# Optimization experiments

Hardware: AMD Instinct MI355X
Metric: run time of the kernel (lower is better)

The kernel has to match this reference:

```python
import math
import jax, jax.numpy as jnp
import numpy as np

N, T, F, H = 30000, 4, 128, 8  # num_node, num_type, num_fea, num_head
D = F // H


def setup_inputs() -> dict:
    key = jax.random.key(0)
    k0, k1, k2, k3, k4 = jax.random.split(key, 5)
    feature = jax.random.normal(k0, (N, F), dtype=jnp.float32)
    edge_fea = jax.random.normal(k1, (N, T, F), dtype=jnp.float32)
    node_multi_mask = jax.random.randint(k2, (N,), 0, T)
    # Xavier-uniform-like scale for [*, F, F] projection tables
    xav = math.sqrt(6.0 / (F + F))
    node_proj = jax.random.uniform(k3, (T, F, F), minval=-xav, maxval=xav, dtype=jnp.float32)
    edge_proj = jax.random.uniform(k4, (T * T, F, F), minval=-xav, maxval=xav, dtype=jnp.float32)
    return {
        "feature": feature,
        "edge_fea": edge_fea,
        "node_multi_mask": node_multi_mask,
        "node_proj": node_proj,
        "edge_proj": edge_proj,
    }


def reference(feature, edge_fea, node_multi_mask, node_proj, edge_proj):
    # Type-indexed projections. Instead of gathering per-node [F,F] matrices
    # (which would materialize N*F*F), compute projections for all T source
    # types in one batched einsum, then select each node's type with a gather.
    # node: out[n] = node_proj[mask[n]] @ feature[n]
    node_all = jnp.einsum('tgf,nf->ntg', node_proj, feature)           # [N,T,F]
    node_p = jnp.take_along_axis(node_all, node_multi_mask[:, None, None], axis=1)[:, 0]  # [N,F]
    # edge: out[n,j] = edge_proj[mask[n]*T + j] @ edge_fea[n,j]
    edge_proj_r = edge_proj.reshape(T, T, F, F)                         # [src_type, j, F, F]
    edge_all = jnp.einsum('stgf,ntf->nstg', edge_proj_r, edge_fea)      # [N,T_src,T,F]
    edge_p = jnp.take_along_axis(edge_all, node_multi_mask[:, None, None, None], axis=1)[:, 0]  # [N,T,F]

    # multi-head attention weights
    node_multi_in = node_p.reshape(N, 1, H, D).transpose(0, 2, 1, 3) / math.sqrt(D)  # [N,H,1,D]
    edge_multi_in = edge_p.reshape(N, T, H, D).transpose(0, 2, 3, 1)                  # [N,H,D,T]
    scores = jnp.matmul(node_multi_in, edge_multi_in)                                 # [N,H,1,T]
    # NOTE: original uses nn.Softmax(dim=1) -> softmax over the HEAD axis
    all_r_weight = jax.nn.softmax(scores, axis=1).transpose(0, 3, 1, 2)               # [N,T,H,1]
    return all_r_weight
```

## Files before the change

### kernel.cpp

```cpp
#include <hip/hip_runtime.h>
#include <hip/hip_bf16.h>

#define N_NODES 30000
#define T_TYPES 4
#define F_DIM   128
#define H_HEADS 8

typedef __bf16 bf16x8 __attribute__((ext_vector_type(8)));
typedef __bf16 bf16x4 __attribute__((ext_vector_type(4)));
typedef float  floatx4 __attribute__((ext_vector_type(4)));

#define WS_NPB 0
#define WS_EPB 131072

template <int CTRL>
static __device__ __forceinline__ float dpp_add(float x) {
    int xi = __builtin_bit_cast(int, x);
    int yi = __builtin_amdgcn_update_dpp(xi, xi, CTRL, 0xF, 0xF, true);
    return x + __builtin_bit_cast(float, yi);
}
static __device__ __forceinline__ float sum16(float x) {
    x = dpp_add<0xB1>(x);
    x = dpp_add<0x4E>(x);
    x = dpp_add<0x141>(x);
    x = dpp_add<0x140>(x);
    return x;
}

__global__ __launch_bounds__(256) void prep_kernel(
    const float* __restrict__ node_proj, const float* __restrict__ edge_proj,
    __bf16* __restrict__ npb, __bf16* __restrict__ epb)
{
    int i = blockIdx.x * 256 + threadIdx.x;
    int base = i * 4;
    float4 v;
    __bf16* dst;
    if (base < T_TYPES * F_DIM * F_DIM) {
        v = ((const float4*)node_proj)[i];
        dst = npb + base;
    } else {
        int off = base - T_TYPES * F_DIM * F_DIM;
        v = ((const float4*)edge_proj)[off >> 2];
        dst = epb + off;
    }
    bf16x4 w = { (__bf16)v.x, (__bf16)v.y, (__bf16)v.z, (__bf16)v.w };
    *(bf16x4*)dst = w;
}

__global__ __launch_bounds__(512, 6) void main_kernel(
    const float* __restrict__ feature, const float* __restrict__ edge_fea,
    const int* __restrict__ mask,
    const __bf16* __restrict__ npb, const __bf16* __restrict__ epb,
    float* __restrict__ out)
{
    const int b = blockIdx.x;
    const int n0 = b * 32;
    const int valid = min(32, N_NODES - n0);

    __shared__ __bf16 Afeat[32][136];
    __shared__ __bf16 Aedge[4][32][136];
    __shared__ float  sc[32][4][H_HEADS + 1];
    __shared__ int    perm[32];
    __shared__ int    tileTy[8], tileOff[8], tileEnd[8];
    __shared__ int    ntilesS;

    const int tid  = threadIdx.x;
    const int lane = tid & 63;
    const int wave = tid >> 6;

    if (wave == 0) {
        int t = (lane < valid) ? mask[n0 + lane] : 99;
        unsigned long long m0 = __ballot(t == 0);
        unsigned long long m1 = __ballot(t == 1);
        unsigned long long m2 = __ballot(t == 2);
        unsigned long long m3 = __ballot(t == 3);
        int c0 = __popcll(m0), c1 = __popcll(m1), c2 = __popcll(m2), c3 = __popcll(m3);
        if (lane < valid && t < 4) {
            unsigned long long mt = (t == 0) ? m0 : (t == 1) ? m1 : (t == 2) ? m2 : m3;
            int base = (t == 0) ? 0 : (t == 1) ? c0 : (t == 2) ? c0 + c1 : c0 + c1 + c2;
            int pos = base + __popcll(mt & ((1ull << lane) - 1ull));
            perm[pos] = lane;
        }
        if (lane == 0) {
            int cnt[4] = {c0, c1, c2, c3};
            int nt = 0, off = 0;
            #pragma unroll
            for (int t4 = 0; t4 < 4; ++t4) {
                int c = cnt[t4], o = off;
                while (c > 0) {
                    tileTy[nt] = t4; tileOff[nt] = o; tileEnd[nt] = off + cnt[t4];
                    o += 16; c -= 16; ++nt;
                }
                off += cnt[t4];
            }
            ntilesS = nt;
        }
    }

    const int colv = tid & 31;
    const int rowg = tid >> 5;
    #pragma unroll
    for (int it = 0; it < 2; ++it) {
        int row = it * 16 + rowg;
        int r = min(row, valid - 1);
        float4 v = ((const float4*)(feature + (long)(n0 + r) * F_DIM))[colv];
        bf16x4 w = { (__bf16)v.x, (__bf16)v.y, (__bf16)v.z, (__bf16)v.w };
        *(bf16x4*)(&Afeat[row][0] + colv * 4) = w;
    }
    #pragma unroll
    for (int it = 0; it < 8; ++it) {
        int row = it * 16 + rowg;
        int j = row >> 5, r0 = row & 31;
        int r = min(r0, valid - 1);
        float4 v = ((const float4*)(edge_fea + ((long)(n0 + r) * 4 + j) * F_DIM))[colv];
        bf16x4 w = { (__bf16)v.x, (__bf16)v.y, (__bf16)v.z, (__bf16)v.w };
        *(bf16x4*)(&Aedge[j][r0][0] + colv * 4) = w;
    }
    __syncthreads();

    const int ml   = lane & 15;
    const int quad = lane >> 4;
    const int g0   = wave * 16;
    const int nt   = ntilesS;

    for (int ti = 0; ti < nt; ++ti) {
        const int t   = tileTy[ti];
        const int off = tileOff[ti];
        const int end = tileEnd[ti];
        const int rown = perm[min(off + ml, end - 1)];

        floatx4 accN = {0.f, 0.f, 0.f, 0.f};
        {
            const __bf16* a0 = &Afeat[rown][quad * 8];
            const __bf16* bp = npb + t * (F_DIM * F_DIM) + (g0 + ml) * F_DIM + quad * 8;
            #pragma unroll
            for (int k0 = 0; k0 < 128; k0 += 32) {
                bf16x8 A0 = *(const bf16x8*)(a0 + k0);
                bf16x8 B0 = *(const bf16x8*)(bp + k0);
                accN = __builtin_amdgcn_mfma_f32_16x16x32_bf16(A0, B0, accN, 0, 0, 0);
            }
        }

        #pragma unroll
        for (int j = 0; j < 4; ++j) {
            floatx4 accE = {0.f, 0.f, 0.f, 0.f};
            const __bf16* a0 = &Aedge[j][rown][quad * 8];
            const __bf16* bp = epb + (t * 4 + j) * (F_DIM * F_DIM) + (g0 + ml) * F_DIM + quad * 8;
            #pragma unroll
            for (int k0 = 0; k0 < 128; k0 += 32) {
                bf16x8 A0 = *(const bf16x8*)(a0 + k0);
                bf16x8 B0 = *(const bf16x8*)(bp + k0);
                accE = __builtin_amdgcn_mfma_f32_16x16x32_bf16(A0, B0, accE, 0, 0, 0);
            }
            floatx4 p = accN * accE;
            p.x = sum16(p.x);
            p.y = sum16(p.y);
            p.z = sum16(p.z);
            p.w = sum16(p.w);
            if (ml == 0) {
                int p0 = off + quad * 4;
                if (p0 + 0 < end) sc[perm[p0 + 0]][j][wave] = p.x * 0.25f;
                if (p0 + 1 < end) sc[perm[p0 + 1]][j][wave] = p.y * 0.25f;
                if (p0 + 2 < end) sc[perm[p0 + 2]][j][wave] = p.z * 0.25f;
                if (p0 + 3 < end) sc[perm[p0 + 3]][j][wave] = p.w * 0.25f;
            }
        }
    }
    __syncthreads();

    if (tid < 128) {
        int node = tid >> 2, j = tid & 3;
        if (node < valid) {
            float v[8], m = -1e30f;
            #pragma unroll
            for (int h = 0; h < 8; ++h) { v[h] = sc[node][j][h]; m = fmaxf(m, v[h]); }
            float s = 0.f;
            #pragma unroll
            for (int h = 0; h < 8; ++h) { v[h] = __expf(v[h] - m); s += v[h]; }
            float r = 1.0f / s;
            float* o = out + (long)(n0 + node) * (T_TYPES * H_HEADS) + j * H_HEADS;
            float4 o0 = { v[0] * r, v[1] * r, v[2] * r, v[3] * r };
            float4 o1 = { v[4] * r, v[5] * r, v[6] * r, v[7] * r };
            ((float4*)o)[0] = o0;
            ((float4*)o)[1] = o1;
        }
    }
}

extern "C" void kernel_launch(void* const* d_in, const int* in_sizes, int n_in,
                              void* d_out, int out_size, void* d_ws, size_t ws_size,
                              hipStream_t stream) {
    const float* feature   = (const float*)d_in[0];
    const float* edge_fea  = (const float*)d_in[1];
    const int*   mask      = (const int*)d_in[2];
    const float* node_proj = (const float*)d_in[3];
    const float* edge_proj = (const float*)d_in[4];
    float* out = (float*)d_out;

    char* ws = (char*)d_ws;
    __bf16* npb = (__bf16*)(ws + WS_NPB);
    __bf16* epb = (__bf16*)(ws + WS_EPB);

    prep_kernel<<<320, 256, 0, stream>>>(node_proj, edge_proj, npb, epb);
    int nblk = (N_NODES + 31) / 32;
    main_kernel<<<nblk, 512, 0, stream>>>(feature, edge_fea, mask, npb, epb, out);
}
```

Baseline: 174.4 us.

## Compute type permutation per wave in registers and prefetch projection fragments

Every wave now computes the type-sorted permutation itself with ballots and a ds_permute, replacing the shared-memory perm/tile tables that wave 0 built. Scores are stored in sorted order and remapped through posS in the softmax. The tile loop becomes an unrolled per-type lambda that loads all B fragments up front and prefetches the next edge projection's weights while the current MFMAs run, to hide global-load latency. The occupancy hint drops from 6 to 4, so the compiler gets more registers for the prefetched fragments but fewer waves may be resident.

```diff
diff --git a/kernel.cpp b/kernel.cpp
--- a/kernel.cpp
+++ b/kernel.cpp
@@ -47,7 +47,7 @@
     *(bf16x4*)dst = w;
 }
 
-__global__ __launch_bounds__(512, 6) void main_kernel(
+__global__ __launch_bounds__(512, 4) void main_kernel(
     const float* __restrict__ feature, const float* __restrict__ edge_fea,
     const int* __restrict__ mask,
     const __bf16* __restrict__ npb, const __bf16* __restrict__ epb,
@@ -60,42 +60,28 @@
     __shared__ __bf16 Afeat[32][136];
     __shared__ __bf16 Aedge[4][32][136];
     __shared__ float  sc[32][4][H_HEADS + 1];
-    __shared__ int    perm[32];
-    __shared__ int    tileTy[8], tileOff[8], tileEnd[8];
-    __shared__ int    ntilesS;
+    __shared__ int    posS[32];
 
     const int tid  = threadIdx.x;
     const int lane = tid & 63;
     const int wave = tid >> 6;
 
-    if (wave == 0) {
-        int t = (lane < valid) ? mask[n0 + lane] : 99;
-        unsigned long long m0 = __ballot(t == 0);
-        unsigned long long m1 = __ballot(t == 1);
-        unsigned long long m2 = __ballot(t == 2);
-        unsigned long long m3 = __ballot(t == 3);
-        int c0 = __popcll(m0), c1 = __popcll(m1), c2 = __popcll(m2), c3 = __popcll(m3);
-        if (lane < valid && t < 4) {
-            unsigned long long mt = (t == 0) ? m0 : (t == 1) ? m1 : (t == 2) ? m2 : m3;
-            int base = (t == 0) ? 0 : (t == 1) ? c0 : (t == 2) ? c0 + c1 : c0 + c1 + c2;
-            int pos = base + __popcll(mt & ((1ull << lane) - 1ull));
-            perm[pos] = lane;
-        }
-        if (lane == 0) {
-            int cnt[4] = {c0, c1, c2, c3};
-            int nt = 0, off = 0;
-            #pragma unroll
-            for (int t4 = 0; t4 < 4; ++t4) {
-                int c = cnt[t4], o = off;
-                while (c > 0) {
-                    tileTy[nt] = t4; tileOff[nt] = o; tileEnd[nt] = off + cnt[t4];
-                    o += 16; c -= 16; ++nt;
-                }
-                off += cnt[t4];
-            }
-            ntilesS = nt;
-        }
-    }
+    int t = 99;
+    if (lane < valid) t = mask[n0 + lane];
+    unsigned long long m0 = __ballot(t == 0);
+    unsigned long long m1 = __ballot(t == 1);
+    unsigned long long m2 = __ballot(t == 2);
+    unsigned long long m3 = __ballot(t == 3);
+    const int c0 = __popcll(m0), c1 = __popcll(m1), c2 = __popcll(m2), c3 = __popcll(m3);
+    const int off0 = 0, off1 = c0, off2 = c0 + c1, off3 = c0 + c1 + c2;
+    int pos = 64 + lane;
+    if (t < 4) {
+        unsigned long long mt = (t == 0) ? m0 : (t == 1) ? m1 : (t == 2) ? m2 : m3;
+        int base = (t == 0) ? off0 : (t == 1) ? off1 : (t == 2) ? off2 : off3;
+        pos = base + __popcll(mt & ((1ull << lane) - 1ull));
+    }
+    const int permv = __builtin_amdgcn_ds_permute(pos << 2, lane);
+    if (wave == 0 && t < 4) posS[lane] = pos;
 
     const int colv = tid & 31;
     const int rowg = tid >> 5;
@@ -121,59 +107,86 @@
     const int ml   = lane & 15;
     const int quad = lane >> 4;
     const int g0   = wave * 16;
-    const int nt   = ntilesS;
-
-    for (int ti = 0; ti < nt; ++ti) {
-        const int t   = tileTy[ti];
-        const int off = tileOff[ti];
-        const int end = tileEnd[ti];
-        const int rown = perm[min(off + ml, end - 1)];
+
+    auto frag = [&](int tt, int o, int c) __attribute__((always_inline)) {
+        const int idx  = o + min(ml, c - 1);
+        const int rown = __builtin_amdgcn_ds_bpermute(idx << 2, permv);
+
+        const __bf16* bpn  = npb + tt * (F_DIM * F_DIM) + (g0 + ml) * F_DIM + quad * 8;
+        const __bf16* bpe0 = epb + (tt * 4) * (F_DIM * F_DIM) + (g0 + ml) * F_DIM + quad * 8;
+        bf16x8 Bn0 = *(const bf16x8*)(bpn +  0);
+        bf16x8 Bn1 = *(const bf16x8*)(bpn + 32);
+        bf16x8 Bn2 = *(const bf16x8*)(bpn + 64);
+        bf16x8 Bn3 = *(const bf16x8*)(bpn + 96);
+        bf16x8 Be0 = *(const bf16x8*)(bpe0 +  0);
+        bf16x8 Be1 = *(const bf16x8*)(bpe0 + 32);
+        bf16x8 Be2 = *(const bf16x8*)(bpe0 + 64);
+        bf16x8 Be3 = *(const bf16x8*)(bpe0 + 96);
+
+        const __bf16* an = &Afeat[rown][quad * 8];
+        bf16x8 Af0 = *(const bf16x8*)(an +  0);
+        bf16x8 Af1 = *(const bf16x8*)(an + 32);
+        bf16x8 Af2 = *(const bf16x8*)(an + 64);
+        bf16x8 Af3 = *(const bf16x8*)(an + 96);
 
         floatx4 accN = {0.f, 0.f, 0.f, 0.f};
-        {
-            const __bf16* a0 = &Afeat[rown][quad * 8];
-            const __bf16* bp = npb + t * (F_DIM * F_DIM) + (g0 + ml) * F_DIM + quad * 8;
-            #pragma unroll
-            for (int k0 = 0; k0 < 128; k0 += 32) {
-                bf16x8 A0 = *(const bf16x8*)(a0 + k0);
-                bf16x8 B0 = *(const bf16x8*)(bp + k0);
-                accN = __builtin_amdgcn_mfma_f32_16x16x32_bf16(A0, B0, accN, 0, 0, 0);
-            }
-        }
+        accN = __builtin_amdgcn_mfma_f32_16x16x32_bf16(Af0, Bn0, accN, 0, 0, 0);
+        accN = __builtin_amdgcn_mfma_f32_16x16x32_bf16(Af1, Bn1, accN, 0, 0, 0);
+        accN = __builtin_amdgcn_mfma_f32_16x16x32_bf16(Af2, Bn2, accN, 0, 0, 0);
+        accN = __builtin_amdgcn_mfma_f32_16x16x32_bf16(Af3, Bn3, accN, 0, 0, 0);
 
         #pragma unroll
         for (int j = 0; j < 4; ++j) {
+            bf16x8 Bf0, Bf1, Bf2, Bf3;
+            if (j < 3) {
+                const __bf16* bpf = bpe0 + (j + 1) * (F_DIM * F_DIM);
+                Bf0 = *(const bf16x8*)(bpf +  0);
+                Bf1 = *(const bf16x8*)(bpf + 32);
+                Bf2 = *(const bf16x8*)(bpf + 64);
+                Bf3 = *(const bf16x8*)(bpf + 96);
+            }
+            const __bf16* ae = &Aedge[j][rown][quad * 8];
+            bf16x8 Ae0 = *(const bf16x8*)(ae +  0);
+            bf16x8 Ae1 = *(const bf16x8*)(ae + 32);
+            bf16x8 Ae2 = *(const bf16x8*)(ae + 64);
+            bf16x8 Ae3 = *(const bf16x8*)(ae + 96);
             floatx4 accE = {0.f, 0.f, 0.f, 0.f};
-            const __bf16* a0 = &Aedge[j][rown][quad * 8];
-            const __bf16* bp = epb + (t * 4 + j) * (F_DIM * F_DIM) + (g0 + ml) * F_DIM + quad * 8;
-            #pragma unroll
-            for (int k0 = 0; k0 < 128; k0 += 32) {
-                bf16x8 A0 = *(const bf16x8*)(a0 + k0);
-                bf16x8 B0 = *(const bf16x8*)(bp + k0);
-                accE = __builtin_amdgcn_mfma_f32_16x16x32_bf16(A0, B0, accE, 0, 0, 0);
-            }
+            accE = __builtin_amdgcn_mfma_f32_16x16x32_bf16(Ae0, Be0, accE, 0, 0, 0);
+            accE = __builtin_amdgcn_mfma_f32_16x16x32_bf16(Ae1, Be1, accE, 0, 0, 0);
+            accE = __builtin_amdgcn_mfma_f32_16x16x32_bf16(Ae2, Be2, accE, 0, 0, 0);
+            accE = __builtin_amdgcn_mfma_f32_16x16x32_bf16(Ae3, Be3, accE, 0, 0, 0);
+
             floatx4 p = accN * accE;
             p.x = sum16(p.x);
             p.y = sum16(p.y);
             p.z = sum16(p.z);
             p.w = sum16(p.w);
             if (ml == 0) {
-                int p0 = off + quad * 4;
-                if (p0 + 0 < end) sc[perm[p0 + 0]][j][wave] = p.x * 0.25f;
-                if (p0 + 1 < end) sc[perm[p0 + 1]][j][wave] = p.y * 0.25f;
-                if (p0 + 2 < end) sc[perm[p0 + 2]][j][wave] = p.z * 0.25f;
-                if (p0 + 3 < end) sc[perm[p0 + 3]][j][wave] = p.w * 0.25f;
+                int q4 = quad * 4;
+                if (q4 + 0 < c) sc[o + q4 + 0][j][wave] = p.x * 0.25f;
+                if (q4 + 1 < c) sc[o + q4 + 1][j][wave] = p.y * 0.25f;
+                if (q4 + 2 < c) sc[o + q4 + 2][j][wave] = p.z * 0.25f;
+                if (q4 + 3 < c) sc[o + q4 + 3][j][wave] = p.w * 0.25f;
             }
+            if (j < 3) { Be0 = Bf0; Be1 = Bf1; Be2 = Bf2; Be3 = Bf3; }
         }
+    };
+
+    {
+        if (c0 > 0) { frag(0, off0, min(c0, 16)); if (c0 > 16) frag(0, off0 + 16, c0 - 16); }
+        if (c1 > 0) { frag(1, off1, min(c1, 16)); if (c1 > 16) frag(1, off1 + 16, c1 - 16); }
+        if (c2 > 0) { frag(2, off2, min(c2, 16)); if (c2 > 16) frag(2, off2 + 16, c2 - 16); }
+        if (c3 > 0) { frag(3, off3, min(c3, 16)); if (c3 > 16) frag(3, off3 + 16, c3 - 16); }
     }
     __syncthreads();
 
     if (tid < 128) {
         int node = tid >> 2, j = tid & 3;
         if (node < valid) {
+            int p = posS[node];
             float v[8], m = -1e30f;
             #pragma unroll
-            for (int h = 0; h < 8; ++h) { v[h] = sc[node][j][h]; m = fmaxf(m, v[h]); }
+            for (int h = 0; h < 8; ++h) { v[h] = sc[p][j][h]; m = fmaxf(m, v[h]); }
             float s = 0.f;
             #pragma unroll
             for (int h = 0; h < 8; ++h) { v[h] = __expf(v[h] - m); s += v[h]; }
```

After: 172.0 us. No clear change (-1.4%).
